# Kernel tuning notes

Hardware: AMD Instinct MI355X
Metric: run time of the kernel (lower is better)

Reference implementation:

```python
import jax, jax.numpy as jnp
import numpy as np

N_NODES = 20000
N_EDGES = 240000
N_GRAPHS = 200
D_IN = 118
H = 256          # simplified hidden width standing in for the mul=50 irreps hidden
NB = 10          # number_of_basis
RH = 100         # fc_neurons hidden
L = 3            # layers
SH = 9           # lmax=2 -> 1+3+5 spherical-harmonic channels
MAX_RADIUS = 5.0
NUM_NEIGHBORS = 12.0


def setup_inputs() -> dict:
    key = jax.random.key(0)
    ks = jax.random.split(key, 16)
    inp = {
        "x": jax.random.normal(ks[0], (N_NODES, D_IN), jnp.float32),
        "pos": jax.random.normal(ks[1], (N_NODES, 3), jnp.float32),
        "edge_shift": jax.random.normal(ks[2], (N_EDGES, 3), jnp.float32),
        "lattice": jax.random.normal(ks[3], (N_GRAPHS, 3, 3), jnp.float32),
        "W_embed": jax.random.normal(ks[4], (D_IN, H), jnp.float32) / np.sqrt(D_IN),
        "r1": jax.random.normal(ks[5], (L, NB, RH), jnp.float32) / np.sqrt(NB),
        "b1": jax.random.normal(ks[6], (L, RH), jnp.float32) * 0.1,
        "r2": jax.random.normal(ks[7], (L, RH, H), jnp.float32) / np.sqrt(RH),
        "Wtp": jax.random.normal(ks[8], (L, SH, H, H), jnp.float32) / np.sqrt(SH * H),
        "Wself": jax.random.normal(ks[9], (L, H, H), jnp.float32) / np.sqrt(H),
        "Wskip": jax.random.normal(ks[10], (L, H, H), jnp.float32) / np.sqrt(H),
        "Wout": jax.random.normal(ks[11], (H, 1), jnp.float32) / np.sqrt(H),
        "edge_index": jax.random.randint(ks[12], (2, N_EDGES), 0, N_NODES, jnp.int64)
                        if jax.config.jax_enable_x64 else
                      jax.random.randint(ks[12], (2, N_EDGES), 0, N_NODES).astype(jnp.int32),
        "batch": jnp.sort(jax.random.randint(ks[13], (N_NODES,), 0, N_GRAPHS)).astype(jnp.int32),
    }
    return inp


def _sph_harm_lmax2(u):
    """Component-normalized real spherical harmonics up to l=2 on unit vectors u [E,3]."""
    x, y, z = u[:, 0], u[:, 1], u[:, 2]
    c1 = np.sqrt(3.0)
    c2 = np.sqrt(15.0)
    return jnp.stack([
        jnp.ones_like(x),                       # l=0
        c1 * x, c1 * y, c1 * z,                 # l=1
        c2 * x * y, c2 * y * z,                 # l=2
        (np.sqrt(5.0) / 2.0) * (3.0 * z * z - 1.0),
        c2 * x * z, (c2 / 2.0) * (x * x - y * y),
    ], axis=1)                                  # [E, 9]


def _soft_one_hot_cosine(lens):
    """e3nn soft_one_hot_linspace(basis='cosine', cutoff=True) * sqrt(NB)."""
    vals = jnp.linspace(0.0, MAX_RADIUS, NB + 2)
    step = vals[1] - vals[0]
    vals = vals[1:-1]
    diff = (lens[:, None] - vals[None, :]) / step          # [E, NB]
    emb = jnp.cos(0.5 * jnp.pi * diff) * (diff > -1.0) * (diff < 1.0)
    return emb * np.sqrt(float(NB))


def _forward(x, pos, edge_shift, lattice, W_embed, r1, b1, r2, Wtp, Wself, Wskip, Wout,
             edge_src, edge_dst, batch):
    edge_batch = batch[edge_src]                            # [E]
    # periodic edge vectors: pos[dst] - pos[src] + shift @ lattice[graph]
    edge_vec = pos[edge_dst] - pos[edge_src] + jnp.einsum(
        'ni,nij->nj', edge_shift, lattice[edge_batch])      # [E, 3]
    lens = jnp.linalg.norm(edge_vec, axis=1)                # [E]
    u = edge_vec / (lens[:, None] + 1e-12)
    sh = _sph_harm_lmax2(u)                                 # [E, 9]
    emb = _soft_one_hot_cosine(lens)                        # [E, NB]

    h = x @ W_embed                                         # [N, H]
    inv_sqrt_deg = 1.0 / np.sqrt(NUM_NEIGHBORS)
    for l in range(L):
        radial = jax.nn.silu(emb @ r1[l] + b1[l]) @ r2[l]   # [E, H]
        hs = h[edge_src] * radial                           # gather + radial gate
        # weighted tensor-product-like message: sum_a (hs * sh_a) @ Wtp[l, a]
        msg = (hs * sh[:, 0:1]) @ Wtp[l, 0]
        for a in range(1, SH):
            msg = msg + (hs * sh[:, a:a + 1]) @ Wtp[l, a]   # [E, H]
        agg = jax.ops.segment_sum(msg, edge_dst, num_segments=N_NODES) * inv_sqrt_deg
        h = jax.nn.gelu(agg @ Wself[l] + h @ Wskip[l])      # [N, H]

    node_out = h @ Wout                                     # [N, 1]
    # scatter_mean over graphs
    sums = jax.ops.segment_sum(node_out, batch, num_segments=N_GRAPHS)
    cnts = jax.ops.segment_sum(jnp.ones((N_NODES, 1), node_out.dtype), batch,
                               num_segments=N_GRAPHS)
    return sums / jnp.maximum(cnts, 1.0)                    # [G, 1]


def reference(x, pos, edge_shift, lattice, W_embed, r1, b1, r2, Wtp, Wself, Wskip, Wout,
              edge_index, batch):
    return _forward(x, pos, edge_shift, lattice, W_embed, r1, b1, r2, Wtp, Wself, Wskip,
                    Wout, edge_index[0], edge_index[1], batch)
```

## Files before the change

### kernel.cpp

```cpp
#include <hip/hip_runtime.h>
#include <hip/hip_bf16.h>
#include <cstddef>
#include <cstdint>

#define NNODE  20000
#define MPAD   20096
#define NEDGE  240000
#define NGRAPH 200
#define DIN    118
#define HD     256
#define NBASIS 10
#define RHID   100
#define NLAYER 3
#define NSH    9
#define SHSTR  16
#define KTP    (NSH * HD)
#define KTOT   (KTP + HD)
#define KR2    128
#define KEMB   128
#define NRT    (MPAD / 64)

typedef _Float16 f16;
typedef _Float16 f16x2 __attribute__((ext_vector_type(2)));
typedef _Float16 f16x4 __attribute__((ext_vector_type(4)));
typedef _Float16 f16x8 __attribute__((ext_vector_type(8)));
typedef float    f32x4 __attribute__((ext_vector_type(4)));

__device__ __forceinline__ float gelu_tanh(float v) {
  float v3 = v * v * v;
  return 0.5f * v * (1.f + tanhf(0.7978845608028654f * (v + 0.044715f * v3)));
}

__device__ __forceinline__ void gload16(const void* g, void* l) {
  __builtin_amdgcn_global_load_lds(
      (const __attribute__((address_space(1))) unsigned int*)g,
      (__attribute__((address_space(3))) unsigned int*)l, 16, 0, 0);
}

__device__ __forceinline__ int perm64(int rho) {
  return (rho & ~63) | ((rho & 15) * 4 + ((rho >> 4) & 3));
}
__device__ __forceinline__ int inv_perm64(int n) {
  return (n & ~63) | (((n & 3) << 4) | ((n >> 2) & 15));
}

__global__ void deg_hist_kernel(const int* __restrict__ ei, int* __restrict__ deg)
{
  int e = blockIdx.x * 256 + threadIdx.x;
  if (e >= NEDGE) return;
  atomicAdd(&deg[ei[NEDGE + e]], 1);
}

__global__ void scan_kernel(const int* __restrict__ deg, int* __restrict__ rowptr)
{
  __shared__ int part[256];
  int t = threadIdx.x;
  const int chunk = (NNODE + 255) / 256;
  int start = t * chunk;
  int end = min(start + chunk, NNODE);
  int s = 0;
  for (int i = start; i < end; ++i) s += deg[i];
  part[t] = s;
  __syncthreads();
  for (int off = 1; off < 256; off <<= 1) {
    int v = (t >= off) ? part[t - off] : 0;
    __syncthreads();
    part[t] += v;
    __syncthreads();
  }
  int run = (t == 0) ? 0 : part[t - 1];
  for (int i = start; i < end; ++i) { rowptr[i] = run; run += deg[i]; }
  if (t == 255) rowptr[NNODE] = run;
}

__global__ void group_build_kernel(const int* __restrict__ rowptr,
                                   int* __restrict__ grp_start,
                                   int* __restrict__ n_groups)
{
  __shared__ int cnts[256];
  int t = threadIdx.x;
  const int chunk = (NNODE + 255) / 256;
  int nbeg = t * chunk;
  int nend = min(nbeg + chunk, NNODE);
  int cnt = 0;
  if (nbeg < nend) {
    int ebase = rowptr[nbeg];
    for (int n = nbeg; n < nend; ++n) {
      if (rowptr[n + 1] - ebase > 64) { ++cnt; ebase = rowptr[n]; }
    }
    ++cnt;
  }
  cnts[t] = cnt;
  __syncthreads();
  for (int off = 1; off < 256; off <<= 1) {
    int v = (t >= off) ? cnts[t - off] : 0;
    __syncthreads();
    cnts[t] += v;
    __syncthreads();
  }
  int g = (t == 0) ? 0 : cnts[t - 1];
  if (nbeg < nend) {
    int ebase = rowptr[nbeg];
    int gstart = nbeg;
    for (int n = nbeg; n < nend; ++n) {
      if (rowptr[n + 1] - ebase > 64) {
        grp_start[g++] = gstart;
        gstart = n;
        ebase = rowptr[n];
      }
    }
    grp_start[g++] = gstart;
  }
  if (t == 255) { grp_start[cnts[255]] = NNODE; *n_groups = cnts[255]; }
}

__global__ void edge_geom_kernel(const float* __restrict__ pos,
                                 const float* __restrict__ shift,
                                 const float* __restrict__ lat,
                                 const int* __restrict__ ei,
                                 const int* __restrict__ batch,
                                 const int* __restrict__ rowptr,
                                 int* __restrict__ cursor,
                                 f16* __restrict__ sh_s,
                                 float* __restrict__ lens_s)
{
  int e = blockIdx.x * 256 + threadIdx.x;
  if (e >= NEDGE) return;
  int src = ei[e];
  int dst = ei[NEDGE + e];
  int b = batch[src];
  const float* L = lat + (size_t)b * 9;
  float s0 = shift[e * 3 + 0], s1 = shift[e * 3 + 1], s2 = shift[e * 3 + 2];
  float ev[3];
#pragma unroll
  for (int j = 0; j < 3; ++j)
    ev[j] = pos[dst * 3 + j] - pos[src * 3 + j] + s0 * L[j] + s1 * L[3 + j] + s2 * L[6 + j];
  float len = sqrtf(ev[0] * ev[0] + ev[1] * ev[1] + ev[2] * ev[2]);
  float inv = 1.f / (len + 1e-12f);
  float x = ev[0] * inv, y = ev[1] * inv, z = ev[2] * inv;
  const float c1 = 1.7320508075688772f;
  const float c2 = 3.872983346207417f;
  int p = atomicAdd(&cursor[dst], 1);
  int si = rowptr[dst] + p;
  f16* she = sh_s + (size_t)si * SHSTR;
  she[0] = (f16)1.f;
  she[1] = (f16)(c1 * x);
  she[2] = (f16)(c1 * y);
  she[3] = (f16)(c1 * z);
  she[4] = (f16)(c2 * x * y);
  she[5] = (f16)(c2 * y * z);
  she[6] = (f16)(1.1180339887498949f * (3.f * z * z - 1.f));
  she[7] = (f16)(c2 * x * z);
  she[8] = (f16)(1.9364916731037085f * (x * x - y * y));
  she[9] = (f16)0.f;
  *(int*)(she + 10) = src;
  she[12] = (f16)0.f; she[13] = (f16)0.f; she[14] = (f16)0.f; she[15] = (f16)0.f;
  lens_s[si] = len;
}

__global__ void prep_kernel(const float* __restrict__ Wtp_l,
                            const float* __restrict__ Wself_l,
                            const float* __restrict__ Wskip_l,
                            const float* __restrict__ r2l,
                            const float* __restrict__ r1l,
                            const float* __restrict__ b1l,
                            f16* __restrict__ Wtp16,
                            f16* __restrict__ WselfT16,
                            f16* __restrict__ Bcat,
                            f16* __restrict__ r2h,
                            f16* __restrict__ r1h)
{
  int b = blockIdx.x, t = threadIdx.x;
  if (b < KTP) {
    int i = b * 256 + t;
    Wtp16[i] = (f16)Wtp_l[i];
  } else if (b < KTP + 256) {
    int n = b - KTP;
    WselfT16[(size_t)n * HD + t] = (f16)(Wself_l[(size_t)t * HD + n] * 0.28867513459481287f);
  } else if (b < KTP + 512) {
    int rho = b - KTP - 256;
    int pcol = perm64(rho);
    Bcat[(size_t)rho * KTOT + KTP + t] = (f16)Wskip_l[(size_t)t * HD + pcol];
  } else if (b < KTP + 768) {
    int rho = b - KTP - 512;
    if (t < KR2) {
      int p = perm64(rho);
      r2h[(size_t)rho * KR2 + t] = (t < RHID) ? (f16)r2l[(size_t)t * HD + p] : (f16)0.f;
    }
  } else {
#pragma unroll
    for (int u = 0; u < 16; ++u) {
      int idx = u * 256 + t;
      int n = idx >> 5, j = idx & 31;
      float v = 0.f;
      if (n < RHID) {
        if (j < NBASIS) v = r1l[(size_t)j * RHID + n];
        else if (j == NBASIS) v = b1l[n];
      }
      r1h[idx] = (f16)v;
    }
  }
}

__global__ void convert_x_kernel(const float* __restrict__ x, f16* __restrict__ xh)
{
  int i = blockIdx.x * 2 + (threadIdx.x >> 7);
  int k = threadIdx.x & 127;
  xh[(size_t)i * KEMB + k] = (i < NNODE && k < DIN) ? (f16)x[(size_t)i * DIN + k] : (f16)0.f;
}

__global__ void convert_wemb_kernel(const float* __restrict__ Wemb, f16* __restrict__ WembT16)
{
  int n = blockIdx.x, k = threadIdx.x;
  WembT16[(size_t)n * KEMB + k] = (k < DIN) ? (f16)Wemb[(size_t)k * HD + n] : (f16)0.f;
}

__global__ __launch_bounds__(256) void gemm_nt_kernel(
    const f16* __restrict__ A, const f16* __restrict__ B,
    f16* __restrict__ C, int K, int ldc, int permRows)
{
  __shared__ __align__(16) f16 As[4][64][8];
  __shared__ __align__(16) f16 Bs[4][128][8];
  int t = threadIdx.x;
  int lane = t & 63, w = t >> 6;
  int row0 = blockIdx.x * 64;
  int n0 = blockIdx.y * 128;
  f32x4 acc[2][4];
#pragma unroll
  for (int i = 0; i < 2; ++i)
#pragma unroll
    for (int j = 0; j < 4; ++j) acc[i][j] = (f32x4){0.f, 0.f, 0.f, 0.f};
  int mq = (w & 1) * 32, nq = (w >> 1) * 64;
  for (int k0 = 0; k0 < K; k0 += 32) {
    {
      int row = t & 63, cc = t >> 6;
      *(uint4*)&As[cc][row][0] = *(const uint4*)(A + (size_t)(row0 + row) * K + k0 + cc * 8);
    }
#pragma unroll
    for (int u = 0; u < 2; ++u) {
      int idx = t + u * 256;
      int ch = idx >> 7, nn = idx & 127;
      *(uint4*)&Bs[ch][nn][0] = *(const uint4*)(B + (size_t)(n0 + nn) * K + k0 + ch * 8);
    }
    __syncthreads();
    int q = lane >> 4, r = lane & 15;
    f16x8 af[2], bfr[4];
#pragma unroll
    for (int i = 0; i < 2; ++i) af[i] = *(const f16x8*)&As[q][mq + i * 16 + r][0];
#pragma unroll
    for (int j = 0; j < 4; ++j) bfr[j] = *(const f16x8*)&Bs[q][nq + j * 16 + r][0];
#pragma unroll
    for (int i = 0; i < 2; ++i)
#pragma unroll
      for (int j = 0; j < 4; ++j)
        acc[i][j] = __builtin_amdgcn_mfma_f32_16x16x32_f16(af[i], bfr[j], acc[i][j], 0, 0, 0);
    __syncthreads();
  }
  int q4 = ((lane >> 4)) * 4, cl = lane & 15;
#pragma unroll
  for (int i = 0; i < 2; ++i)
#pragma unroll
    for (int rr = 0; rr < 4; ++rr) {
      int row = row0 + mq + i * 16 + q4 + rr;
      int orow = permRows ? inv_perm64(row) : row;
#pragma unroll
      for (int j = 0; j < 4; ++j)
        C[(size_t)orow * ldc + n0 + nq + j * 16 + cl] = (f16)acc[i][j][rr];
    }
}

#define RHSTR 136
#define HSSTR 264
__global__ __launch_bounds__(256) void radial_gather_kernel(
    const int* __restrict__ rowptr,
    const int* __restrict__ grp_start,
    const int* __restrict__ n_groups,
    const float* __restrict__ lens_s,
    const f16* __restrict__ sh_s,
    const f16* __restrict__ h,
    const f16* __restrict__ r1h,
    const f16* __restrict__ r2h,
    f16* __restrict__ T)
{
  __shared__ __align__(16) char smem[64 * HSSTR * 2];
  __shared__ int srcs[64];
  __shared__ __align__(16) f16 shL[64][16];
  f16* emb_s = (f16*)smem;
  f16* rhA   = (f16*)(smem + 64 * 40 * 2);
  f16* hs_s  = (f16*)smem;

  int t = threadIdx.x;
  int lane = t & 63, w = t >> 6;
  int r = lane & 15, q = lane >> 4;
  int half = t >> 7, lc = t & 127;
  int n0w = w * 64;

  f16x8 bfr[4][4];
#pragma unroll
  for (int j = 0; j < 4; ++j)
#pragma unroll
    for (int ks = 0; ks < 4; ++ks)
      bfr[j][ks] = *(const f16x8*)(r2h + (size_t)(n0w + j * 16 + r) * KR2 + ks * 32 + q * 8);
  f16x8 b1f[2];
#pragma unroll
  for (int j = 0; j < 2; ++j)
    b1f[j] = *(const f16x8*)(r1h + (size_t)((2 * w + j) * 16 + r) * 32 + q * 8);

  int ng = *n_groups;
  for (int g = blockIdx.x; g < ng; g += gridDim.x) {
    int gn0 = grp_start[g], gn1 = grp_start[g + 1];
    int ebeg = rowptr[gn0];

    {
      int e = ebeg + (t >> 2); if (e >= NEDGE) e = NEDGE - 1;
      *(f16x4*)&shL[t >> 2][(t & 3) * 4] = *(const f16x4*)(sh_s + (size_t)e * SHSTR + (t & 3) * 4);
    }
    if (t < 64) {
      int e = ebeg + t; if (e >= NEDGE) e = NEDGE - 1;
      srcs[t] = *(const int*)(sh_s + (size_t)e * SHSTR + 10);
    }

    {
      int le = ebeg + lane; if (le >= NEDGE) le = NEDGE - 1;
      float len = lens_s[le];
      const float step = 5.f / 11.f;
      const float sq = 3.1622776601683795f;
      f16x8 v;
#pragma unroll
      for (int kk = 0; kk < 8; ++kk) {
        int j = w * 8 + kk;
        float val = 0.f;
        if (j < NBASIS) {
          float d = (len - (float)(j + 1) * step) / step;
          val = (d > -1.f && d < 1.f) ? (__cosf(1.5707963267948966f * d) * sq) : 0.f;
        } else if (j == NBASIS) {
          val = 1.f;
        }
        v[kk] = (f16)val;
      }
      *(f16x8*)&emb_s[lane * 40 + w * 8] = v;
    }
    __syncthreads();

    f32x4 acc1[4][2];
#pragma unroll
    for (int i = 0; i < 4; ++i)
#pragma unroll
      for (int j = 0; j < 2; ++j) acc1[i][j] = (f32x4){0.f, 0.f, 0.f, 0.f};
    {
      f16x8 a1f[4];
#pragma unroll
      for (int i = 0; i < 4; ++i)
        a1f[i] = *(const f16x8*)&emb_s[(i * 16 + r) * 40 + q * 8];
#pragma unroll
      for (int i = 0; i < 4; ++i)
#pragma unroll
        for (int j = 0; j < 2; ++j)
          acc1[i][j] = __builtin_amdgcn_mfma_f32_16x16x32_f16(a1f[i], b1f[j], acc1[i][j], 0, 0, 0);
    }

#pragma unroll
    for (int i = 0; i < 4; ++i)
#pragma unroll
      for (int j = 0; j < 2; ++j)
#pragma unroll
        for (int rr = 0; rr < 4; ++rr) {
          float s = acc1[i][j][rr];
          s = __fdividef(s, 1.f + __expf(-s));
          rhA[(i * 16 + q * 4 + rr) * RHSTR + (2 * w + j) * 16 + r] = (f16)s;
        }
    __syncthreads();

    f16x4 hv[4][4];
#pragma unroll
    for (int i = 0; i < 4; ++i)
#pragma unroll
      for (int rr = 0; rr < 4; ++rr) {
        int m = i * 16 + q * 4 + rr;
        hv[i][rr] = *(const f16x4*)(h + (size_t)srcs[m] * HD + n0w + r * 4);
      }

    f32x4 acc[4][4];
#pragma unroll
    for (int i = 0; i < 4; ++i)
#pragma unroll
      for (int j = 0; j < 4; ++j) acc[i][j] = (f32x4){0.f, 0.f, 0.f, 0.f};
#pragma unroll
    for (int ks = 0; ks < 4; ++ks) {
      f16x8 af[4];
#pragma unroll
      for (int i = 0; i < 4; ++i)
        af[i] = *(const f16x8*)&rhA[(i * 16 + r) * RHSTR + ks * 32 + q * 8];
#pragma unroll
      for (int i = 0; i < 4; ++i)
#pragma unroll
        for (int j = 0; j < 4; ++j)
          acc[i][j] = __builtin_amdgcn_mfma_f32_16x16x32_f16(af[i], bfr[j][ks], acc[i][j], 0, 0, 0);
    }
    __syncthreads();

#pragma unroll
    for (int i = 0; i < 4; ++i)
#pragma unroll
      for (int rr = 0; rr < 4; ++rr) {
        int m = i * 16 + q * 4 + rr;
        f16x4 o;
#pragma unroll
        for (int j = 0; j < 4; ++j)
          o[j] = (f16)(acc[i][j][rr] * (float)hv[i][rr][j]);
        *(f16x4*)&hs_s[m * HSSTR + n0w + r * 4] = o;
      }
    __syncthreads();

    int npair = (gn1 - gn0 + 1) >> 1;
    for (int s = 0; s < npair; ++s) {
      int n = gn0 + s * 2 + half;
      if (n < gn1) {
        int beg = rowptr[n] - ebeg, end = rowptr[n + 1] - ebeg;
        float a0[NSH], a1[NSH];
#pragma unroll
        for (int a = 0; a < NSH; ++a) { a0[a] = 0.f; a1[a] = 0.f; }
        for (int j = beg; j < end; ++j) {
          f16x2 rv = *(const f16x2*)&hs_s[j * HSSTR + 2 * lc];
          float p0 = (float)rv[0], p1 = (float)rv[1];
          f16x8 s8 = *(const f16x8*)&shL[j][0];
          float s8v = (float)shL[j][8];
#pragma unroll
          for (int a = 0; a < 8; ++a) {
            float sv = (float)s8[a];
            a0[a] += sv * p0;
            a1[a] += sv * p1;
          }
          a0[8] += s8v * p0;
          a1[8] += s8v * p1;
        }
        f16* Tn = T + (size_t)n * KTP + 2 * lc;
#pragma unroll
        for (int a = 0; a < NSH; ++a) {
          f16x2 o; o[0] = (f16)a0[a]; o[1] = (f16)a1[a];
          *(f16x2*)(Tn + a * HD) = o;
        }
      }
    }
    __syncthreads();
  }
}

#define GBM 64
#define GBN 128
#define NKSTEP (KTOT / 32)
__global__ __launch_bounds__(256) void gemm_fused_kernel(
    const f16* __restrict__ A1,
    const f16* __restrict__ A2,
    const f16* __restrict__ B,
    f16* __restrict__ C)
{
  __shared__ __align__(16) f16 As[2][GBM][4][8];
  __shared__ __align__(16) f16 Bs[2][GBN][4][8];
  int t = threadIdx.x;
  int lane = t & 63, w = t >> 6;
  int row0 = blockIdx.x * GBM;
  int n0 = blockIdx.y * GBN;
  int mq = (w & 1) * 32, nq = (w >> 1) * 64;
  int arow = t >> 2, ach = t & 3;

  f32x4 acc[2][4];
#pragma unroll
  for (int i = 0; i < 2; ++i)
#pragma unroll
    for (int j = 0; j < 4; ++j) acc[i][j] = (f32x4){0.f, 0.f, 0.f, 0.f};

  auto stage = [&](int buf, int k0) {
    const f16* ga = (k0 < KTP)
        ? (A1 + (size_t)(row0 + arow) * KTP + k0 + ach * 8)
        : (A2 + (size_t)(row0 + arow) * HD + (k0 - KTP) + ach * 8);
    gload16(ga, &As[buf][0][0][0] + (size_t)w * 512);
#pragma unroll
    for (int u = 0; u < 2; ++u) {
      int idx = t + u * 256;
      const f16* gb = B + (size_t)(n0 + (idx >> 2)) * KTOT + k0 + (idx & 3) * 8;
      gload16(gb, &Bs[buf][0][0][0] + (size_t)(u * 256 + w * 64) * 8);
    }
  };

  stage(0, 0);
  __syncthreads();

  int cur = 0;
  int q = lane >> 4, r = lane & 15;
  for (int s = 0; s < NKSTEP; ++s) {
    if (s + 1 < NKSTEP) stage(cur ^ 1, (s + 1) * 32);
    f16x8 af[2], bfr[4];
#pragma unroll
    for (int i = 0; i < 2; ++i) af[i] = *(const f16x8*)&As[cur][mq + i * 16 + r][q][0];
#pragma unroll
    for (int j = 0; j < 4; ++j) bfr[j] = *(const f16x8*)&Bs[cur][nq + j * 16 + r][q][0];
#pragma unroll
    for (int i = 0; i < 2; ++i)
#pragma unroll
      for (int j = 0; j < 4; ++j)
        acc[i][j] = __builtin_amdgcn_mfma_f32_16x16x32_f16(af[i], bfr[j], acc[i][j], 0, 0, 0);
    __syncthreads();
    cur ^= 1;
  }

  int q4 = (lane >> 4) * 4, cl = lane & 15;
#pragma unroll
  for (int i = 0; i < 2; ++i)
#pragma unroll
    for (int rr = 0; rr < 4; ++rr) {
      int row = row0 + mq + i * 16 + q4 + rr;
      f16x4 o;
#pragma unroll
      for (int j = 0; j < 4; ++j) o[j] = (f16)gelu_tanh(acc[i][j][rr]);
      *(f16x4*)(C + (size_t)row * HD + n0 + nq + cl * 4) = o;
    }
}

__global__ __launch_bounds__(256) void node_out_fused_kernel(
    const f16* __restrict__ h,
    const float* __restrict__ Wout,
    const int* __restrict__ batch,
    float* __restrict__ out)
{
  __shared__ float red[256];
  int g = blockIdx.x;
  int t = threadIdx.x;
  int lo = 0, hi = NNODE;
  while (lo < hi) { int mid = (lo + hi) >> 1; if (batch[mid] < g) lo = mid + 1; else hi = mid; }
  int start = lo;
  hi = NNODE;
  while (lo < hi) { int mid = (lo + hi) >> 1; if (batch[mid] < g + 1) lo = mid + 1; else hi = mid; }
  int end = lo;
  int half = t >> 7, lc = t & 127;
  float a0 = 0.f, a1 = 0.f;
  for (int n = start + half; n < end; n += 2) {
    f16x2 v = *(const f16x2*)(h + (size_t)n * HD + 2 * lc);
    a0 += (float)v[0];
    a1 += (float)v[1];
  }
  red[t] = a0 * Wout[2 * lc] + a1 * Wout[2 * lc + 1];
  for (int off = 128; off > 0; off >>= 1) {
    __syncthreads();
    if (t < off) red[t] += red[t + off];
  }
  if (t == 0) out[g] = red[0] / fmaxf((float)(end - start), 1.f);
}

extern "C" void kernel_launch(void* const* d_in, const int* in_sizes, int n_in,
                              void* d_out, int out_size, void* d_ws, size_t ws_size,
                              hipStream_t stream)
{
  (void)in_sizes; (void)n_in; (void)out_size;
  const float* x     = (const float*)d_in[0];
  const float* pos   = (const float*)d_in[1];
  const float* shift = (const float*)d_in[2];
  const float* lat   = (const float*)d_in[3];
  const float* Wemb  = (const float*)d_in[4];
  const float* r1    = (const float*)d_in[5];
  const float* b1    = (const float*)d_in[6];
  const float* r2    = (const float*)d_in[7];
  const float* Wtp   = (const float*)d_in[8];
  const float* Wself = (const float*)d_in[9];
  const float* Wskip = (const float*)d_in[10];
  const float* Wout  = (const float*)d_in[11];
  const int*   eidx  = (const int*)d_in[12];
  const int*   batch = (const int*)d_in[13];
  float* out = (float*)d_out;

  char* ws = (char*)d_ws;
  size_t off = 0;
  auto alloc = [&](size_t bytes) -> char* {
    char* p = ws + off;
    off += (bytes + 255) & ~(size_t)255;
    return p;
  };
  f16*   sh_s    = (f16*)alloc((size_t)NEDGE * SHSTR * 2);
  float* lens_s  = (float*)alloc((size_t)NEDGE * 4);
  f16*   hA      = (f16*)alloc((size_t)MPAD * HD * 2);
  f16*   hB      = (f16*)alloc((size_t)MPAD * HD * 2);
  f16*   T       = (f16*)alloc((size_t)MPAD * KTP * 2);
  f16*   rad     = (f16*)alloc((size_t)MPAD * KEMB * 2 + (size_t)HD * KEMB * 2);
  f16*   Bcat    = (f16*)alloc((size_t)HD * KTOT * 2);
  f16*   r2h     = (f16*)alloc((size_t)HD * KR2 * 2);
  f16*   r1hb    = (f16*)alloc((size_t)128 * 32 * 2);
  f16*   Wtp16   = (f16*)alloc((size_t)KTP * HD * 2);
  f16*   WselfT16= (f16*)alloc((size_t)HD * HD * 2);
  int*   rowptr  = (int*)alloc((size_t)(NNODE + 1) * 4);
  int*   deg     = (int*)alloc((size_t)NNODE * 4);
  int*   cursor  = (int*)alloc((size_t)NNODE * 4);
  int*   grp     = (int*)alloc((size_t)(NNODE + 2) * 4);
  int*   ngrp    = (int*)alloc(256);
  if (off > ws_size) return;

  f16*   xh      = rad;
  f16*   WembT16 = rad + (size_t)MPAD * KEMB;

  hipMemsetAsync(deg, 0, (size_t)NNODE * 4, stream);
  hipMemsetAsync(cursor, 0, (size_t)NNODE * 4, stream);

  const int EB = (NEDGE + 255) / 256;
  deg_hist_kernel<<<EB, 256, 0, stream>>>(eidx, deg);
  scan_kernel<<<1, 256, 0, stream>>>(deg, rowptr);
  group_build_kernel<<<1, 256, 0, stream>>>(rowptr, grp, ngrp);
  edge_geom_kernel<<<EB, 256, 0, stream>>>(pos, shift, lat, eidx, batch,
                                           rowptr, cursor, sh_s, lens_s);

  convert_x_kernel<<<MPAD / 2, 256, 0, stream>>>(x, xh);
  convert_wemb_kernel<<<HD, KEMB, 0, stream>>>(Wemb, WembT16);
  {
    dim3 eg(MPAD / 64, HD / 128);
    gemm_nt_kernel<<<eg, 256, 0, stream>>>(xh, WembT16, hA, KEMB, HD, 0);
  }

  f16* hcur = hA;
  f16* hnxt = hB;
  dim3 fgrid(NRT, 2);
  dim3 wgrid(HD / 64, KTP / 128);
  for (int l = 0; l < NLAYER; ++l) {
    const float* r1l = r1 + (size_t)l * NBASIS * RHID;
    const float* b1l = b1 + (size_t)l * RHID;
    const float* r2l = r2 + (size_t)l * RHID * HD;
    const float* Wtp_l = Wtp + (size_t)l * NSH * HD * HD;
    const float* Wself_l = Wself + (size_t)l * HD * HD;
    const float* Wskip_l = Wskip + (size_t)l * HD * HD;

    prep_kernel<<<KTP + 768 + 1, 256, 0, stream>>>(Wtp_l, Wself_l, Wskip_l, r2l,
                                                   r1l, b1l,
                                                   Wtp16, WselfT16, Bcat, r2h, r1hb);
    gemm_nt_kernel<<<wgrid, 256, 0, stream>>>(WselfT16, Wtp16, Bcat, HD, KTOT, 1);

    radial_gather_kernel<<<4608, 256, 0, stream>>>(rowptr, grp, ngrp, lens_s,
                                                   sh_s, hcur, r1hb, r2h, T);
    gemm_fused_kernel<<<fgrid, 256, 0, stream>>>(T, hcur, Bcat, hnxt);
    f16* tmp = hcur; hcur = hnxt; hnxt = tmp;
  }

  node_out_fused_kernel<<<NGRAPH, 256, 0, stream>>>(hcur, Wout, batch, out);
}
```

Before: 764.3 us.

## Replace scalar per-node SH aggregation with MFMA using block-sparse SH weight matrix

The radial_gather kernel now builds a 64x64 selector matrix in shared memory holding each edge's spherical-harmonic coefficients at rows (local node, channel). It multiplies that matrix by a transposed gated-message tile with MFMA, replacing the scalar per-node edge loop that accumulated 9 channels in FP32 registers. Group building is capped at 7 nodes per group so that 9 channels per node fit in 64 output rows. The trade-offs are more groups, an extra shared-memory zeroing pass per group, a smaller transposed shared buffer written with scalar stores, and a launch-bounds occupancy hint.

```diff
diff --git a/kernel.cpp b/kernel.cpp
--- a/kernel.cpp
+++ b/kernel.cpp
@@ -85,8 +85,11 @@
   int cnt = 0;
   if (nbeg < nend) {
     int ebase = rowptr[nbeg];
+    int gstart = nbeg;
     for (int n = nbeg; n < nend; ++n) {
-      if (rowptr[n + 1] - ebase > 64) { ++cnt; ebase = rowptr[n]; }
+      if (rowptr[n + 1] - ebase > 64 || n - gstart >= 7) {
+        ++cnt; ebase = rowptr[n]; gstart = n;
+      }
     }
     ++cnt;
   }
@@ -103,7 +106,7 @@
     int ebase = rowptr[nbeg];
     int gstart = nbeg;
     for (int n = nbeg; n < nend; ++n) {
-      if (rowptr[n + 1] - ebase > 64) {
+      if (rowptr[n + 1] - ebase > 64 || n - gstart >= 7) {
         grp_start[g++] = gstart;
         gstart = n;
         ebase = rowptr[n];
@@ -270,8 +273,8 @@
 }
 
 #define RHSTR 136
-#define HSSTR 264
-__global__ __launch_bounds__(256) void radial_gather_kernel(
+#define ESTE  66
+__global__ __launch_bounds__(256, 3) void radial_gather_kernel(
     const int* __restrict__ rowptr,
     const int* __restrict__ grp_start,
     const int* __restrict__ n_groups,
@@ -282,17 +285,20 @@
     const f16* __restrict__ r2h,
     f16* __restrict__ T)
 {
-  __shared__ __align__(16) char smem[64 * HSSTR * 2];
+  __shared__ __align__(16) char smem[(256 + 64) * ESTE * 2];
+  __shared__ __align__(16) f16 shL[64][16];
   __shared__ int srcs[64];
-  __shared__ __align__(16) f16 shL[64][16];
+  __shared__ int ln_s[64];
+  __shared__ signed char m2n_s[64];
+  __shared__ signed char m2a_s[64];
   f16* emb_s = (f16*)smem;
   f16* rhA   = (f16*)(smem + 64 * 40 * 2);
-  f16* hs_s  = (f16*)smem;
+  f16* hs_t  = (f16*)smem;
+  f16* Wp    = (f16*)(smem + 256 * ESTE * 2);
 
   int t = threadIdx.x;
   int lane = t & 63, w = t >> 6;
   int r = lane & 15, q = lane >> 4;
-  int half = t >> 7, lc = t & 127;
   int n0w = w * 64;
 
   f16x8 bfr[4][4];
@@ -310,7 +316,16 @@
   for (int g = blockIdx.x; g < ng; g += gridDim.x) {
     int gn0 = grp_start[g], gn1 = grp_start[g + 1];
     int ebeg = rowptr[gn0];
-
+    int ecnt = rowptr[gn1] - ebeg;
+
+    {
+      uint4 z = {0u, 0u, 0u, 0u};
+#pragma unroll
+      for (int u = 0; u < 3; ++u) {
+        int idx = u * 256 + t;
+        if (idx < (64 * ESTE * 2) / 16) ((uint4*)Wp)[idx] = z;
+      }
+    }
     {
       int e = ebeg + (t >> 2); if (e >= NEDGE) e = NEDGE - 1;
       *(f16x4*)&shL[t >> 2][(t & 3) * 4] = *(const f16x4*)(sh_s + (size_t)e * SHSTR + (t & 3) * 4);
@@ -318,6 +333,12 @@
     if (t < 64) {
       int e = ebeg + t; if (e >= NEDGE) e = NEDGE - 1;
       srcs[t] = *(const int*)(sh_s + (size_t)e * SHSTR + 10);
+      int ln = 0;
+      while (gn0 + ln + 1 < gn1 && ebeg + t >= rowptr[gn0 + ln + 1]) ++ln;
+      ln_s[t] = ln;
+      int nn = gn1 - gn0;
+      m2n_s[t] = (t < 9 * nn) ? (signed char)(t / 9) : (signed char)(-1);
+      m2a_s[t] = (signed char)(t % 9);
     }
 
     {
@@ -342,6 +363,16 @@
     }
     __syncthreads();
 
+    {
+      int e = t >> 2, p = t & 3;
+      if (e < ecnt) {
+        int mb = ln_s[e] * 9;
+        Wp[(mb + p) * ESTE + e]     = shL[e][p];
+        Wp[(mb + 4 + p) * ESTE + e] = shL[e][4 + p];
+        if (p == 0) Wp[(mb + 8) * ESTE + e] = shL[e][8];
+      }
+    }
+
     f32x4 acc1[4][2];
 #pragma unroll
     for (int i = 0; i < 4; ++i)
@@ -402,46 +433,50 @@
 #pragma unroll
     for (int i = 0; i < 4; ++i)
 #pragma unroll
+      for (int j = 0; j < 4; ++j)
+#pragma unroll
+        for (int rr = 0; rr < 4; ++rr) {
+          int m = i * 16 + q * 4 + rr;
+          hs_t[(n0w + j * 16 + r) * ESTE + m] =
+              (f16)(acc[i][j][rr] * (float)hv[i][rr][j]);
+        }
+    __syncthreads();
+
+    f32x4 og[4][4];
+#pragma unroll
+    for (int i = 0; i < 4; ++i)
+#pragma unroll
+      for (int j = 0; j < 4; ++j) og[i][j] = (f32x4){0.f, 0.f, 0.f, 0.f};
+#pragma unroll
+    for (int ks = 0; ks < 2; ++ks) {
+      f16x8 af[4], bf[4];
+#pragma unroll
+      for (int i = 0; i < 4; ++i)
+        af[i] = *(const f16x8*)&Wp[(i * 16 + r) * ESTE + ks * 32 + q * 8];
+#pragma unroll
+      for (int j = 0; j < 4; ++j)
+        bf[j] = *(const f16x8*)&hs_t[(n0w + j * 16 + r) * ESTE + ks * 32 + q * 8];
+#pragma unroll
+      for (int i = 0; i < 4; ++i)
+#pragma unroll
+        for (int j = 0; j < 4; ++j)
+          og[i][j] = __builtin_amdgcn_mfma_f32_16x16x32_f16(af[i], bf[j], og[i][j], 0, 0, 0);
+    }
+
+#pragma unroll
+    for (int i = 0; i < 4; ++i)
+#pragma unroll
       for (int rr = 0; rr < 4; ++rr) {
         int m = i * 16 + q * 4 + rr;
-        f16x4 o;
-#pragma unroll
-        for (int j = 0; j < 4; ++j)
-          o[j] = (f16)(acc[i][j][rr] * (float)hv[i][rr][j]);
-        *(f16x4*)&hs_s[m * HSSTR + n0w + r * 4] = o;
-      }
-    __syncthreads();
-
-    int npair = (gn1 - gn0 + 1) >> 1;
-    for (int s = 0; s < npair; ++s) {
-      int n = gn0 + s * 2 + half;
-      if (n < gn1) {
-        int beg = rowptr[n] - ebeg, end = rowptr[n + 1] - ebeg;
-        float a0[NSH], a1[NSH];
-#pragma unroll
-        for (int a = 0; a < NSH; ++a) { a0[a] = 0.f; a1[a] = 0.f; }
-        for (int j = beg; j < end; ++j) {
-          f16x2 rv = *(const f16x2*)&hs_s[j * HSSTR + 2 * lc];
-          float p0 = (float)rv[0], p1 = (float)rv[1];
-          f16x8 s8 = *(const f16x8*)&shL[j][0];
-          float s8v = (float)shL[j][8];
-#pragma unroll
-          for (int a = 0; a < 8; ++a) {
-            float sv = (float)s8[a];
-            a0[a] += sv * p0;
-            a1[a] += sv * p1;
-          }
-          a0[8] += s8v * p0;
-          a1[8] += s8v * p1;
+        int nd = m2n_s[m];
+        if (nd >= 0) {
+          int a = m2a_s[m];
+          f16x4 o;
+#pragma unroll
+          for (int j = 0; j < 4; ++j) o[j] = (f16)og[i][j][rr];
+          *(f16x4*)(T + (size_t)(gn0 + nd) * KTP + a * HD + n0w + r * 4) = o;
         }
-        f16* Tn = T + (size_t)n * KTP + 2 * lc;
-#pragma unroll
-        for (int a = 0; a < NSH; ++a) {
-          f16x2 o; o[0] = (f16)a0[a]; o[1] = (f16)a1[a];
-          *(f16x2*)(Tn + a * HD) = o;
-        }
-      }
-    }
+      }
     __syncthreads();
   }
 }
```

After: 994.7 us. +30.2%, slower.
